# Performance work log

Hardware: AMD Instinct MI355X
Metric: run time of the kernel (lower is better)

Reference implementation:

```python
import jax, jax.numpy as jnp
import numpy as np

IN_F = 4096
OUT_F = 8192
BLOCK = 16   # block_dim
KEEP = 8     # keep_k low-frequency modes kept per block
NLEV = 256   # n_levels


def dct_inv_basis(keep_k, n):
    # Orthonormal DCT-II synthesis basis, rows = kept frequencies k, cols = time index t.
    k = jnp.arange(keep_k, dtype=jnp.float32)[:, None]
    t = jnp.arange(n, dtype=jnp.float32)[None, :]
    B = jnp.cos(jnp.pi * (t + 0.5) * k / n) * jnp.sqrt(2.0 / n)
    scale = jnp.where(jnp.arange(keep_k) == 0, 1.0 / jnp.sqrt(2.0), 1.0)
    return B * scale[:, None]  # [keep_k, block_dim]


def setup_inputs() -> dict:
    key = jax.random.key(0)
    k1, k2, k3, k4, k5 = jax.random.split(key, 5)
    n_blocks = OUT_F * IN_F // BLOCK  # 2097152
    x = jax.random.normal(k1, (32, 8, IN_F), jnp.float32)
    idx = jax.random.randint(k2, (n_blocks, KEEP), 0, NLEV, jnp.int32)
    c_min = jax.random.normal(k3, (KEEP,), jnp.float32)
    c_range = jax.random.uniform(k4, (KEEP,), jnp.float32) + 0.1
    bias = jax.random.normal(k5, (OUT_F,), jnp.float32)
    return {"x": x, "idx": idx, "c_min": c_min, "c_range": c_range, "bias": bias}


def reference(x, idx, c_min, c_range, bias):
    # Affine dequant of kept frequency codes: [n_blocks, keep_k]
    coeffs = idx.astype(jnp.float32) / (NLEV - 1) * c_range + c_min
    # Inverse DCT per block (high-frequency modes are implicitly zero)
    B = dct_inv_basis(KEEP, BLOCK)              # [keep_k, block_dim]
    W = (coeffs @ B).reshape(OUT_F, IN_F)       # dense dequantized weight
    return x @ W.T + bias
```

## Files before the change

### kernel.cpp

```cpp
#include <hip/hip_runtime.h>


typedef __attribute__((ext_vector_type(8))) short bf16x8;
typedef __attribute__((ext_vector_type(4))) float f32x4;

#define K_TOT   2048
#define N_TOT   8192
#define NT      32
#define NCHUNK  8
#define SPC     8
#define LDS_CH  16384

__device__ __forceinline__ unsigned short f2bf_rn(float f) {
    unsigned u = __float_as_uint(f);
    u += 0x7FFFu + ((u >> 16) & 1u);
    return (unsigned short)(u >> 16);
}
__device__ __forceinline__ unsigned pack2(int a, int b) {
    unsigned ua = __float_as_uint((float)a);
    unsigned ub = __float_as_uint((float)b);
    return __builtin_amdgcn_perm(ub, ua, 0x07060302u);
}

__device__ __forceinline__ void lds_barrier() {
    asm volatile("" ::: "memory");
    __builtin_amdgcn_s_waitcnt(0xC07F);
    __builtin_amdgcn_s_barrier();
    asm volatile("" ::: "memory");
}

__global__ __launch_bounds__(256) void prep_kernel(
    const float* __restrict__ x, const float* __restrict__ c_min,
    const float* __restrict__ c_range, unsigned short* __restrict__ Y2f,
    float* __restrict__ corr)
{
    __shared__ float Bk[8][16];
    __shared__ float scmin[8];
    __shared__ float ss[8];
    __shared__ float red[4];
    const int tid = threadIdx.x;
    const int m = blockIdx.x;
    if (tid < 128) {
        int k = tid >> 4, t = tid & 15;
        float v = cosf(3.14159265358979f * (t + 0.5f) * (float)k / 16.0f)
                  * 0.353553390593274f;
        if (k == 0) v *= 0.707106781186548f;
        Bk[k][t] = v;
    }
    if (tid < 8) {
        scmin[tid] = c_min[tid];
        ss[tid] = c_range[tid] * (1.0f / 255.0f);
    }
    __syncthreads();

    const float* xp = x + (long)m * 4096 + tid * 16;
    float xs[16];
#pragma unroll
    for (int q = 0; q < 4; ++q) {
        float4 v = *(const float4*)(xp + q * 4);
        xs[q * 4 + 0] = v.x; xs[q * 4 + 1] = v.y;
        xs[q * 4 + 2] = v.z; xs[q * 4 + 3] = v.w;
    }
    float partial = 0.0f;
    unsigned short yo[8];
#pragma unroll
    for (int k = 0; k < 8; ++k) {
        float y = 0.0f;
#pragma unroll
        for (int t = 0; t < 16; ++t) y += xs[t] * Bk[k][t];
        partial += y * scmin[k];
        yo[k] = f2bf_rn(y * ss[k]);
    }
    uint4 pk;
    pk.x = (unsigned)yo[0] | ((unsigned)yo[1] << 16);
    pk.y = (unsigned)yo[2] | ((unsigned)yo[3] << 16);
    pk.z = (unsigned)yo[4] | ((unsigned)yo[5] << 16);
    pk.w = (unsigned)yo[6] | ((unsigned)yo[7] << 16);
    {
        const int mg = m >> 4, fr = m & 15, kc = tid >> 2, fq = tid & 3;
        unsigned short* dst = Y2f + ((long)((mg * 64 + kc) * 64) + fq * 16 + fr) * 8;
        *(uint4*)dst = pk;
    }
#pragma unroll
    for (int off = 32; off > 0; off >>= 1)
        partial += __shfl_down(partial, off, 64);
    if ((tid & 63) == 0) red[tid >> 6] = partial;
    __syncthreads();
    if (tid == 0) corr[m] = red[0] + red[1] + red[2] + red[3];
}

__global__ __launch_bounds__(512, 2) void gemm_kernel(
    const unsigned short* __restrict__ Y2f, const int* __restrict__ idx,
    const float* __restrict__ bias, const float* __restrict__ corr,
    float* __restrict__ out)
{
    __shared__ char lds[NCHUNK * LDS_CH];
    __shared__ int flags[NCHUNK][4];

    const int tid  = threadIdx.x;
    const int wave = tid >> 6;
    const int lane = tid & 63;
    const int o0   = blockIdx.x * NT;

    if (tid < NCHUNK * 4) flags[tid >> 2][tid & 3] = 0;

    if (wave >= 4) {
        const int pw   = wave - 4;
        const int col  = pw * 8 + (lane >> 3);
        const int pr0  = lane & 7;
        const int* pBase = idx + (long)(o0 + col) * K_TOT + pr0 * 8;
        char* cBase = lds + col * 512;

        int4 S[2][4][2];
#define PLOAD(slot, ch)                                                   \
        {                                                                 \
            _Pragma("unroll")                                             \
            for (int r = 0; r < 4; ++r) {                                 \
                const int* p = pBase + (ch) * 256 + r * 64;               \
                S[slot][r][0] = *(const int4*)p;                          \
                S[slot][r][1] = *(const int4*)(p + 4);                    \
            }                                                             \
        }
        PLOAD(0, 0)
        PLOAD(1, 1)
        lds_barrier();

#pragma unroll
        for (int c = 0; c < NCHUNK; ++c) {
#pragma unroll
            for (int r = 0; r < 4; ++r) {
                uint4 w;
                w.x = pack2(S[c & 1][r][0].x, S[c & 1][r][0].y);
                w.y = pack2(S[c & 1][r][0].z, S[c & 1][r][0].w);
                w.z = pack2(S[c & 1][r][1].x, S[c & 1][r][1].y);
                w.w = pack2(S[c & 1][r][1].z, S[c & 1][r][1].w);
                *(uint4*)(cBase + c * LDS_CH + (((pr0 + 8 * r) ^ col) * 16)) = w;
            }
            asm volatile("s_waitcnt lgkmcnt(0)" ::: "memory");
            if (lane == 0) *(volatile int*)&flags[c][pw] = 1;
            const int nc = (c + 2 < NCHUNK) ? (c + 2) : (NCHUNK - 1);
            PLOAD(c & 1, nc)
        }
#undef PLOAD
    } else {
        const int fr = lane & 15;
        const int fq = lane >> 4;
        const bf16x8* aF = (const bf16x8*)Y2f + (long)(wave * 4) * 4096 + lane;

        f32x4 acc[4][2];
#pragma unroll
        for (int mt = 0; mt < 4; ++mt)
#pragma unroll
            for (int g = 0; g < 2; ++g)
                acc[mt][g] = (f32x4){0.f, 0.f, 0.f, 0.f};

        bf16x8 a[8][4];
#pragma unroll
        for (int d = 0; d < 8; ++d)
#pragma unroll
            for (int mt = 0; mt < 4; ++mt)
                a[d][mt] = aF[mt * 4096 + d * 64];

        lds_barrier();

#define BREAD(buf, s, g)                                                  \
    (*(const bf16x8*)((buf) + (g * 16 + fr) * 512 +                       \
                      ((((s) * 4 + fq) ^ (g * 16 + fr)) * 16)))

#pragma unroll
        for (int c = 0; c < NCHUNK; ++c) {
            for (;;) {
                int f0 = *(volatile int*)&flags[c][0];
                int f1 = *(volatile int*)&flags[c][1];
                int f2 = *(volatile int*)&flags[c][2];
                int f3 = *(volatile int*)&flags[c][3];
                if (f0 & f1 & f2 & f3) break;
            }
            asm volatile("" ::: "memory");
            const char* buf = lds + c * LDS_CH;
#pragma unroll
            for (int s = 0; s < SPC; ++s) {
                bf16x8 b0 = BREAD(buf, s, 0);
                bf16x8 b1 = BREAD(buf, s, 1);
#pragma unroll
                for (int mt = 0; mt < 4; ++mt) {
                    acc[mt][0] = __builtin_amdgcn_mfma_f32_16x16x32_bf16(
                        a[s][mt], b0, acc[mt][0], 0, 0, 0);
                    acc[mt][1] = __builtin_amdgcn_mfma_f32_16x16x32_bf16(
                        a[s][mt], b1, acc[mt][1], 0, 0, 0);
                }
                {
                    const int nks = (c * SPC + s + 8) & 63;
#pragma unroll
                    for (int mt = 0; mt < 4; ++mt)
                        a[s][mt] = aF[mt * 4096 + nks * 64];
                }
            }
        }
#undef BREAD

#pragma unroll
        for (int mt = 0; mt < 4; ++mt) {
#pragma unroll
            for (int g = 0; g < 2; ++g) {
                const int col = o0 + g * 16 + fr;
                const float bv = bias[col];
                const int row0 = (wave * 4 + mt) * 16 + fq * 4;
#pragma unroll
                for (int r = 0; r < 4; ++r)
                    out[(long)(row0 + r) * N_TOT + col] =
                        acc[mt][g][r] + bv + corr[row0 + r];
            }
        }
    }
}

extern "C" void kernel_launch(void* const* d_in, const int* in_sizes, int n_in,
                              void* d_out, int out_size, void* d_ws, size_t ws_size,
                              hipStream_t stream) {
    const float* x       = (const float*)d_in[0];
    const int*   idx     = (const int*)d_in[1];
    const float* c_min   = (const float*)d_in[2];
    const float* c_range = (const float*)d_in[3];
    const float* bias    = (const float*)d_in[4];
    float* out = (float*)d_out;

    unsigned short* Y2f = (unsigned short*)d_ws;
    float* corr = (float*)((char*)d_ws + (size_t)256 * K_TOT * 2);

    prep_kernel<<<256, 256, 0, stream>>>(x, c_min, c_range, Y2f, corr);
    gemm_kernel<<<256, 512, 0, stream>>>(Y2f, idx, bias, corr, out);
}
```

Before: 120.6 us.

## Stream int codes into LDS via async global_load_lds ring buffer, convert at read

Producer waves now copy raw int32 index codes straight into a 4-slot LDS ring buffer using asynchronous global-to-LDS loads. The int-to-bf16 conversion moves onto the MFMA consumer waves at read time, and consumers signal per-chunk completion so slots can be reused. The workgroup shrinks to 384 threads with 2 producer waves, the A-fragment register prefetch is cut from 8 to 2 steps, and a padded column stride replaces the XOR swizzle. This is meant to remove producer register staging and conversion work. The cost is more LDS traffic per MFMA (double bytes read), conversion ALU on the critical consumer path, and an extra done/flag handshake.

```diff
diff --git a/kernel.cpp b/kernel.cpp
--- a/kernel.cpp
+++ b/kernel.cpp
@@ -9,7 +9,8 @@
 #define NT      32
 #define NCHUNK  8
 #define SPC     8
-#define LDS_CH  16384
+#define COL_STR 1040
+#define REG_SZ  (NT * COL_STR)
 
 __device__ __forceinline__ unsigned short f2bf_rn(float f) {
     unsigned u = __float_as_uint(f);
@@ -20,6 +21,14 @@
     unsigned ua = __float_as_uint((float)a);
     unsigned ub = __float_as_uint((float)b);
     return __builtin_amdgcn_perm(ub, ua, 0x07060302u);
+}
+__device__ __forceinline__ bf16x8 cvt8(int4 lo, int4 hi) {
+    union { unsigned u[4]; bf16x8 v; } r;
+    r.u[0] = pack2(lo.x, lo.y);
+    r.u[1] = pack2(lo.z, lo.w);
+    r.u[2] = pack2(hi.x, hi.y);
+    r.u[3] = pack2(hi.z, hi.w);
+    return r.v;
 }
 
 __device__ __forceinline__ void lds_barrier() {
@@ -27,6 +36,12 @@
     __builtin_amdgcn_s_waitcnt(0xC07F);
     __builtin_amdgcn_s_barrier();
     asm volatile("" ::: "memory");
+}
+
+__device__ __forceinline__ void async16(const int* gp, char* lp) {
+    __builtin_amdgcn_global_load_lds(
+        (const __attribute__((address_space(1))) unsigned int*)gp,
+        (__attribute__((address_space(3))) unsigned int*)lp, 16, 0, 0);
 }
 
 __global__ __launch_bounds__(256) void prep_kernel(
@@ -89,59 +104,61 @@
     if (tid == 0) corr[m] = red[0] + red[1] + red[2] + red[3];
 }
 
-__global__ __launch_bounds__(512, 2) void gemm_kernel(
+__global__ __launch_bounds__(384, 1) void gemm_kernel(
     const unsigned short* __restrict__ Y2f, const int* __restrict__ idx,
     const float* __restrict__ bias, const float* __restrict__ corr,
     float* __restrict__ out)
 {
-    __shared__ char lds[NCHUNK * LDS_CH];
-    __shared__ int flags[NCHUNK][4];
+    __shared__ char lds[4 * REG_SZ];
+    __shared__ int flags[NCHUNK][2];
+    __shared__ int done[NCHUNK][4];
 
     const int tid  = threadIdx.x;
     const int wave = tid >> 6;
     const int lane = tid & 63;
     const int o0   = blockIdx.x * NT;
 
-    if (tid < NCHUNK * 4) flags[tid >> 2][tid & 3] = 0;
+    if (tid < NCHUNK * 2) flags[tid >> 1][tid & 1] = 0;
+    if (tid < NCHUNK * 4) done[tid >> 2][tid & 3] = 0;
 
     if (wave >= 4) {
-        const int pw   = wave - 4;
-        const int col  = pw * 8 + (lane >> 3);
-        const int pr0  = lane & 7;
-        const int* pBase = idx + (long)(o0 + col) * K_TOT + pr0 * 8;
-        char* cBase = lds + col * 512;
-
-        int4 S[2][4][2];
-#define PLOAD(slot, ch)                                                   \
+        const int pw = wave - 4;
+        const int c0 = pw * 16;
+        const int* gBase = idx + (long)(o0 + c0) * K_TOT + lane * 4;
+        char* lBase = lds;
+
+#define STAGE(ch)                                                         \
         {                                                                 \
+            char* reg = lBase + ((ch) & 3) * REG_SZ + c0 * COL_STR;       \
             _Pragma("unroll")                                             \
-            for (int r = 0; r < 4; ++r) {                                 \
-                const int* p = pBase + (ch) * 256 + r * 64;               \
-                S[slot][r][0] = *(const int4*)p;                          \
-                S[slot][r][1] = *(const int4*)(p + 4);                    \
-            }                                                             \
-        }
-        PLOAD(0, 0)
-        PLOAD(1, 1)
+            for (int l = 0; l < 16; ++l)                                  \
+                async16(gBase + (long)l * K_TOT + (ch) * 256,             \
+                        reg + l * COL_STR);                               \
+        }
+
+        STAGE(0)
+        STAGE(1)
         lds_barrier();
 
 #pragma unroll
         for (int c = 0; c < NCHUNK; ++c) {
-#pragma unroll
-            for (int r = 0; r < 4; ++r) {
-                uint4 w;
-                w.x = pack2(S[c & 1][r][0].x, S[c & 1][r][0].y);
-                w.y = pack2(S[c & 1][r][0].z, S[c & 1][r][0].w);
-                w.z = pack2(S[c & 1][r][1].x, S[c & 1][r][1].y);
-                w.w = pack2(S[c & 1][r][1].z, S[c & 1][r][1].w);
-                *(uint4*)(cBase + c * LDS_CH + (((pr0 + 8 * r) ^ col) * 16)) = w;
+            if (c + 2 < NCHUNK) {
+                if (c + 2 >= 4) {
+                    while (!(*(volatile int*)&done[c - 2][0] &
+                             *(volatile int*)&done[c - 2][1] &
+                             *(volatile int*)&done[c - 2][2] &
+                             *(volatile int*)&done[c - 2][3]))
+                        __builtin_amdgcn_s_sleep(1);
+                    asm volatile("" ::: "memory");
+                }
+                STAGE(c + 2)
             }
-            asm volatile("s_waitcnt lgkmcnt(0)" ::: "memory");
+            if (c < NCHUNK - 2)      asm volatile("s_waitcnt vmcnt(32)" ::: "memory");
+            else if (c == NCHUNK - 2) asm volatile("s_waitcnt vmcnt(16)" ::: "memory");
+            else                      asm volatile("s_waitcnt vmcnt(0)"  ::: "memory");
             if (lane == 0) *(volatile int*)&flags[c][pw] = 1;
-            const int nc = (c + 2 < NCHUNK) ? (c + 2) : (NCHUNK - 1);
-            PLOAD(c & 1, nc)
-        }
-#undef PLOAD
+        }
+#undef STAGE
     } else {
         const int fr = lane & 15;
         const int fq = lane >> 4;
@@ -154,50 +171,49 @@
             for (int g = 0; g < 2; ++g)
                 acc[mt][g] = (f32x4){0.f, 0.f, 0.f, 0.f};
 
-        bf16x8 a[8][4];
-#pragma unroll
-        for (int d = 0; d < 8; ++d)
-#pragma unroll
-            for (int mt = 0; mt < 4; ++mt)
-                a[d][mt] = aF[mt * 4096 + d * 64];
+        bf16x8 a[2][4];
+#pragma unroll
+        for (int mt = 0; mt < 4; ++mt) {
+            a[0][mt] = aF[mt * 4096 + 0 * 64];
+            a[1][mt] = aF[mt * 4096 + 1 * 64];
+        }
 
         lds_barrier();
 
-#define BREAD(buf, s, g)                                                  \
-    (*(const bf16x8*)((buf) + (g * 16 + fr) * 512 +                       \
-                      ((((s) * 4 + fq) ^ (g * 16 + fr)) * 16)))
+        const int bo0 = fr * COL_STR + fq * 32;
+        const int bo1 = (16 + fr) * COL_STR + fq * 32;
 
 #pragma unroll
         for (int c = 0; c < NCHUNK; ++c) {
-            for (;;) {
-                int f0 = *(volatile int*)&flags[c][0];
-                int f1 = *(volatile int*)&flags[c][1];
-                int f2 = *(volatile int*)&flags[c][2];
-                int f3 = *(volatile int*)&flags[c][3];
-                if (f0 & f1 & f2 & f3) break;
-            }
+            while (!(*(volatile int*)&flags[c][0] &
+                     *(volatile int*)&flags[c][1]))
+                __builtin_amdgcn_s_sleep(1);
             asm volatile("" ::: "memory");
-            const char* buf = lds + c * LDS_CH;
+            const char* buf = lds + (c & 3) * REG_SZ;
 #pragma unroll
             for (int s = 0; s < SPC; ++s) {
-                bf16x8 b0 = BREAD(buf, s, 0);
-                bf16x8 b1 = BREAD(buf, s, 1);
+                const char* p0 = buf + bo0 + s * 128;
+                const char* p1 = buf + bo1 + s * 128;
+                bf16x8 b0 = cvt8(*(const int4*)p0, *(const int4*)(p0 + 16));
+                bf16x8 b1 = cvt8(*(const int4*)p1, *(const int4*)(p1 + 16));
 #pragma unroll
                 for (int mt = 0; mt < 4; ++mt) {
                     acc[mt][0] = __builtin_amdgcn_mfma_f32_16x16x32_bf16(
-                        a[s][mt], b0, acc[mt][0], 0, 0, 0);
+                        a[s & 1][mt], b0, acc[mt][0], 0, 0, 0);
                     acc[mt][1] = __builtin_amdgcn_mfma_f32_16x16x32_bf16(
-                        a[s][mt], b1, acc[mt][1], 0, 0, 0);
+                        a[s & 1][mt], b1, acc[mt][1], 0, 0, 0);
                 }
                 {
-                    const int nks = (c * SPC + s + 8) & 63;
+                    const int ks = c * SPC + s;
+                    const int nks = (ks + 2 < 64) ? ks + 2 : 63;
 #pragma unroll
                     for (int mt = 0; mt < 4; ++mt)
-                        a[s][mt] = aF[mt * 4096 + nks * 64];
+                        a[s & 1][mt] = aF[mt * 4096 + nks * 64];
                 }
             }
-        }
-#undef BREAD
+            asm volatile("s_waitcnt lgkmcnt(0)" ::: "memory");
+            if (lane == 0) *(volatile int*)&done[c][wave] = 1;
+        }
 
 #pragma unroll
         for (int mt = 0; mt < 4; ++mt) {
@@ -229,5 +245,5 @@
     float* corr = (float*)((char*)d_ws + (size_t)256 * K_TOT * 2);
 
     prep_kernel<<<256, 256, 0, stream>>>(x, c_min, c_range, Y2f, corr);
-    gemm_kernel<<<256, 512, 0, stream>>>(Y2f, idx, bias, corr, out);
-}
+    gemm_kernel<<<256, 384, 0, stream>>>(Y2f, idx, bias, corr, out);
+}
```

Result: slower. 130.5 us (+8.3%).
